# Performance work log

Hardware: AMD Instinct MI355X
Metric: run time of the kernel (lower is better)

The kernel has to match this reference:

```python
import jax, jax.numpy as jnp
import numpy as np

B, T, D = 16, 2048, 1024
TT = T - 2            # tokens after stripping BOS/EOS
WORD_EVERY = 3        # a word starts every 3 BPE tokens
MAX_WORDS = TT // WORD_EVERY  # 682
NUM_MUTEX, NUM_BIN = 64, 32


def setup_inputs() -> dict:
    key = jax.random.key(0)
    ks = jax.random.split(key, 7)
    features = jax.random.normal(ks[0], (B, T, D), dtype=jnp.float32)
    word_starts = jnp.zeros((B, TT), dtype=jnp.int32).at[:, ::WORD_EVERY].set(1)
    s = 1.0 / np.sqrt(D)
    dense_w = jax.random.normal(ks[1], (D, D), dtype=jnp.float32) * s
    dense_b = jax.random.normal(ks[2], (D,), dtype=jnp.float32) * 0.01
    out_w = jax.random.normal(ks[3], (NUM_MUTEX, D), dtype=jnp.float32) * s
    out_b = jax.random.normal(ks[4], (NUM_MUTEX,), dtype=jnp.float32) * 0.01
    bin_w = jax.random.normal(ks[5], (NUM_BIN, D + NUM_MUTEX), dtype=jnp.float32) * s
    bin_b = jax.random.normal(ks[6], (NUM_BIN,), dtype=jnp.float32) * 0.01
    return {"features": features, "word_starts": word_starts,
            "dense_w": dense_w, "dense_b": dense_b,
            "out_w": out_w, "out_b": out_b,
            "bin_w": bin_w, "bin_b": bin_b,
            "max_words": MAX_WORDS}


def _word_features(features, word_starts, max_words):
    # strip BOS/EOS
    x = features[:, 1:-1]                                  # [B, TT, D]
    b, tt, d = x.shape
    seg = jnp.cumsum(word_starts, axis=1) - 1              # word id per token; -1 before first start
    valid = seg >= 0
    flat_seg = seg + jnp.arange(b, dtype=seg.dtype)[:, None] * max_words
    overflow = b * max_words                               # dump invalid tokens into extra bucket
    flat_seg = jnp.where(valid, flat_seg, overflow).reshape(-1)
    sums = jax.ops.segment_sum(x.reshape(-1, d), flat_seg,
                               num_segments=b * max_words + 1)[:-1]
    counts = jax.ops.segment_sum(jnp.ones((b * tt,), dtype=x.dtype), flat_seg,
                                 num_segments=b * max_words + 1)[:-1]
    sums = sums.reshape(b, max_words, d)
    counts = counts.reshape(b, max_words, 1)
    # torch code initializes word_features to ONES; empty slots stay 1.0
    return jnp.where(counts > 0, sums, jnp.ones((), dtype=x.dtype))


def reference(features, word_starts, dense_w, dense_b, out_w, out_b, bin_w, bin_b, max_words):
    wf = _word_features(features, word_starts, max_words)   # [B, MW, D]
    # dropout p=0 (eval) -> identity
    h = jnp.tanh(jnp.einsum('bwd,ed->bwe', wf, dense_w) + dense_b)
    word_class_logits = jnp.einsum('bwd,cd->bwc', h, out_w) + out_b
    cat = jnp.concatenate((word_class_logits, h), axis=-1)  # [B, MW, Cm+D]
    binary_logits = jnp.einsum('bwd,cd->bwc', cat, bin_w) + bin_b
    return (word_class_logits, binary_logits)
```

## Files before the change

kernel.cpp:

```cpp
#include <hip/hip_runtime.h>
#include <stdint.h>

#define B_   16
#define T_   2048
#define D_   1024
#define TT_  2046
#define W_   682
#define BW_  (B_ * W_)
#define NMUT 64
#define NBIN 32

typedef __attribute__((ext_vector_type(8))) short s8b;
typedef __attribute__((ext_vector_type(4))) float f32x4;

__device__ inline short f2bf(float f) {
    uint32_t u = __builtin_bit_cast(uint32_t, f);
    u += 0x7FFFu + ((u >> 16) & 1u);
    return (short)(u >> 16);
}

__device__ inline float fast_tanh(float x) {
    float xc = fminf(fmaxf(x, -15.f), 15.f);
    float e  = __expf(2.f * xc);
    return 1.f - 2.f / (e + 1.f);
}

__device__ inline void gload_lds16(const void* g, void* l) {
    __builtin_amdgcn_global_load_lds(
        (const __attribute__((address_space(1))) uint32_t*)g,
        (__attribute__((address_space(3))) uint32_t*)l, 16, 0, 0);
}

__global__ __launch_bounds__(256) void k_prep(const int* __restrict__ ws,
                                              const float* __restrict__ dw,
                                              const float* __restrict__ ow,
                                              const float* __restrict__ ob,
                                              const float* __restrict__ bw,
                                              const float* __restrict__ bb,
                                              int* __restrict__ starts,
                                              int* __restrict__ nwords,
                                              short* __restrict__ dwb,
                                              short* __restrict__ Bcat,
                                              float* __restrict__ beff) {
    __shared__ float smem[NMUT];
    int blk = blockIdx.x;
    int tid = threadIdx.x;

    if (blk < 16) {
        int b = blk;
        const int* row = ws + (size_t)b * TT_;
        int vals[8], incl[8];
        int p = 0;
        int t0 = tid * 8;
#pragma unroll
        for (int i = 0; i < 8; ++i) {
            int t = t0 + i;
            int v = (t < TT_) ? row[t] : 0;
            vals[i] = v;
            p += v;
            incl[i] = p;
        }
        int tot = p;
        int lane = tid & 63;
        int x = tot;
#pragma unroll
        for (int off = 1; off < 64; off <<= 1) {
            int v = __shfl_up(x, off);
            if (lane >= off) x += v;
        }
        int* wsum = (int*)smem;
        int wid = tid >> 6;
        if (lane == 63) wsum[wid] = x;
        __syncthreads();
        int wbase = 0;
        for (int q = 0; q < wid; ++q) wbase += wsum[q];
        int excl = wbase + x - tot;
        int* st = starts + (size_t)b * (W_ + 1);
#pragma unroll
        for (int i = 0; i < 8; ++i) {
            if (vals[i]) {
                int w = excl + incl[i] - 1;
                if (w <= W_) st[w] = t0 + i;
            }
        }
        if (tid == 0) {
            int total = wsum[0] + wsum[1] + wsum[2] + wsum[3];
            int nw = total < W_ ? total : W_;
            nwords[b] = nw;
            if (total <= W_) st[total] = TT_;
        }
    } else if (blk < 16 + 1024) {
        int i = (blk - 16) * 256 + tid;
        float4 v = ((const float4*)dw)[i];
        short4 o;
        o.x = f2bf(v.x); o.y = f2bf(v.y); o.z = f2bf(v.z); o.w = f2bf(v.w);
        *(short4*)(dwb + (size_t)i * 4) = o;
    } else if (blk < 16 + 1024 + 64) {
        int i = (blk - 1040) * 256 + tid;
        float4 v = ((const float4*)ow)[i];
        short4 o;
        o.x = f2bf(v.x); o.y = f2bf(v.y); o.z = f2bf(v.z); o.w = f2bf(v.w);
        *(short4*)(Bcat + (size_t)i * 4) = o;
    } else {
        int j = blk - 1104;
        if (tid < NMUT) smem[tid] = bw[(size_t)j * (D_ + NMUT) + tid];
        __syncthreads();
        for (int k = tid; k < D_; k += 256) {
            float acc = bw[(size_t)j * (D_ + NMUT) + NMUT + k];
#pragma unroll 8
            for (int c = 0; c < NMUT; ++c)
                acc = fmaf(smem[c], ow[(size_t)c * D_ + k], acc);
            Bcat[(size_t)(NMUT + j) * D_ + k] = f2bf(acc);
        }
        if (tid == 0) {
            float acc = bb[j];
            for (int c = 0; c < NMUT; ++c) acc = fmaf(smem[c], ob[c], acc);
            beff[j] = acc;
        }
    }
}

__global__ __launch_bounds__(256) void k_wf(const float* __restrict__ feat,
                                            const int* __restrict__ starts,
                                            const int* __restrict__ nwords,
                                            short* __restrict__ wf) {
    int blk = blockIdx.x;
    int b = blk / W_;
    int w = blk - b * W_;
    int tid = threadIdx.x;
    short* outp = wf + (size_t)blk * D_ + tid * 4;
    int nw = nwords[b];
    float4 acc = make_float4(0.f, 0.f, 0.f, 0.f);
    if (w >= nw) {
        acc = make_float4(1.f, 1.f, 1.f, 1.f);
    } else {
        const int* st = starts + (size_t)b * (W_ + 1);
        int s = st[w], e = st[w + 1];
        const float4* base = (const float4*)(feat + ((size_t)b * T_ + 1) * D_) + tid;
        for (int t = s; t < e; ++t) {
            float4 v = base[(size_t)t * (D_ / 4)];
            acc.x += v.x; acc.y += v.y; acc.z += v.z; acc.w += v.w;
        }
    }
    short4 o;
    o.x = f2bf(acc.x); o.y = f2bf(acc.y); o.z = f2bf(acc.z); o.w = f2bf(acc.w);
    *(short4*)outp = o;
}

__global__ __launch_bounds__(256) void k_gemm1(const short* __restrict__ wf,
                                               const short* __restrict__ dwb,
                                               const float* __restrict__ db,
                                               short* __restrict__ h) {
    __shared__ short As[2][128 * 32];
    __shared__ short Bs[2][128 * 32];
    int tid  = threadIdx.x;
    int lane = tid & 63;
    int w    = tid >> 6;
    int wm = w >> 1, wn = w & 1;
    int bm = blockIdx.x * 128;
    int bn = blockIdx.y * 128;

    int ln = lane & 15;
    int qk = lane >> 4;

    int srow = lane >> 2;
    int scol = (lane & 3) * 8;

    f32x4 acc[4][4];
#pragma unroll
    for (int i = 0; i < 4; ++i)
#pragma unroll
        for (int j = 0; j < 4; ++j) acc[i][j] = (f32x4){0.f, 0.f, 0.f, 0.f};

    for (int kt = 0; kt < D_; kt += 64) {
#pragma unroll
        for (int hh = 0; hh < 2; ++hh) {
#pragma unroll
            for (int p = 0; p < 2; ++p) {
                int chunk = w * 2 + p;
                int arow = bm + chunk * 16 + srow;
                arow = arow < BW_ ? arow : BW_ - 1;
                gload_lds16(wf + (size_t)arow * D_ + kt + hh * 32 + scol,
                            &As[hh][chunk * 512]);
                int brow = bn + chunk * 16 + srow;
                gload_lds16(dwb + (size_t)brow * D_ + kt + hh * 32 + scol,
                            &Bs[hh][chunk * 512]);
            }
        }
        __syncthreads();
#pragma unroll
        for (int hh = 0; hh < 2; ++hh) {
            s8b af[4], bf[4];
#pragma unroll
            for (int i = 0; i < 4; ++i)
                af[i] = *(const s8b*)&As[hh][(wm * 64 + i * 16 + ln) * 32 + qk * 8];
#pragma unroll
            for (int j = 0; j < 4; ++j)
                bf[j] = *(const s8b*)&Bs[hh][(wn * 64 + j * 16 + ln) * 32 + qk * 8];
#pragma unroll
            for (int i = 0; i < 4; ++i)
#pragma unroll
                for (int j = 0; j < 4; ++j)
                    acc[i][j] = __builtin_amdgcn_mfma_f32_16x16x32_bf16(
                        af[i], bf[j], acc[i][j], 0, 0, 0);
        }
        __syncthreads();
    }

    float bias[4];
#pragma unroll
    for (int j = 0; j < 4; ++j) bias[j] = db[bn + wn * 64 + j * 16 + ln];
#pragma unroll
    for (int i = 0; i < 4; ++i) {
        int row0 = bm + wm * 64 + i * 16 + qk * 4;
#pragma unroll
        for (int r = 0; r < 4; ++r) {
            int row = row0 + r;
            if (row < BW_) {
#pragma unroll
                for (int j = 0; j < 4; ++j) {
                    int cn = bn + wn * 64 + j * 16 + ln;
                    h[(size_t)row * D_ + cn] =
                        f2bf(fast_tanh(acc[i][j][r] + bias[j]));
                }
            }
        }
    }
}

__global__ __launch_bounds__(256) void k_gemm2(const short* __restrict__ h,
                                               const short* __restrict__ Bcat,
                                               const float* __restrict__ ob,
                                               const float* __restrict__ beff,
                                               float* __restrict__ out) {
    int tid  = threadIdx.x;
    int lane = tid & 63;
    int w    = tid >> 6;
    int ln = lane & 15, qk = lane >> 4;
    int m0 = blockIdx.x * 64 + w * 16;

    int arow = m0 + ln;
    arow = arow < BW_ ? arow : BW_ - 1;
    const short* ap = h + (size_t)arow * D_ + qk * 8;
    const short* bp = Bcat + (size_t)ln * D_ + qk * 8;

    f32x4 acc[6];
#pragma unroll
    for (int j = 0; j < 6; ++j) acc[j] = (f32x4){0.f, 0.f, 0.f, 0.f};

#pragma unroll 4
    for (int kt = 0; kt < D_; kt += 32) {
        s8b af = *(const s8b*)(ap + kt);
        s8b bf[6];
#pragma unroll
        for (int j = 0; j < 6; ++j)
            bf[j] = *(const s8b*)(bp + (size_t)j * 16 * D_ + kt);
#pragma unroll
        for (int j = 0; j < 6; ++j)
            acc[j] = __builtin_amdgcn_mfma_f32_16x16x32_bf16(af, bf[j], acc[j], 0, 0, 0);
    }

    float bj[6];
#pragma unroll
    for (int j = 0; j < 6; ++j) {
        int c = j * 16 + ln;
        bj[j] = (c < NMUT) ? ob[c] : beff[c - NMUT];
    }
#pragma unroll
    for (int r = 0; r < 4; ++r) {
        int row = m0 + qk * 4 + r;
        if (row < BW_) {
#pragma unroll
            for (int j = 0; j < 6; ++j) {
                int c = j * 16 + ln;
                float v = acc[j][r] + bj[j];
                if (c < NMUT) out[(size_t)row * NMUT + c] = v;
                else out[(size_t)BW_ * NMUT + (size_t)row * NBIN + (c - NMUT)] = v;
            }
        }
    }
}

extern "C" void kernel_launch(void* const* d_in, const int* in_sizes, int n_in,
                              void* d_out, int out_size, void* d_ws, size_t ws_size,
                              hipStream_t stream) {
    const float* feat    = (const float*)d_in[0];
    const int*   wstarts = (const int*)d_in[1];
    const float* dw      = (const float*)d_in[2];
    const float* db      = (const float*)d_in[3];
    const float* ow      = (const float*)d_in[4];
    const float* ob      = (const float*)d_in[5];
    const float* bw      = (const float*)d_in[6];
    const float* bb      = (const float*)d_in[7];
    float* out = (float*)d_out;

    char* ws = (char*)d_ws;
    size_t off = 0;
    auto alloc = [&](size_t bytes) {
        void* p = ws + off;
        off += (bytes + 255) & ~(size_t)255;
        return p;
    };
    short* wf     = (short*)alloc((size_t)BW_ * D_ * 2);
    short* h      = (short*)alloc((size_t)BW_ * D_ * 2);
    short* dwb    = (short*)alloc((size_t)D_ * D_ * 2);
    short* Bcat   = (short*)alloc((size_t)(NMUT + NBIN) * D_ * 2);
    float* beff   = (float*)alloc(NBIN * 4);
    int*   starts = (int*)alloc((size_t)B_ * (W_ + 1) * 4);
    int*   nwords = (int*)alloc(B_ * 4);

    k_prep<<<1136, 256, 0, stream>>>(wstarts, dw, ow, ob, bw, bb,
                                     starts, nwords, dwb, Bcat, beff);
    k_wf<<<BW_, 256, 0, stream>>>(feat, starts, nwords, wf);
    k_gemm1<<<dim3((BW_ + 127) / 128, D_ / 128), 256, 0, stream>>>(wf, dwb, db, h);
    k_gemm2<<<(BW_ + 63) / 64, 256, 0, stream>>>(h, Bcat, ob, beff, out);
}
```

Baseline: 283.8 us.

## Fuse second GEMM into first GEMM epilogue via LDS tile and atomic accumulation

The tanh tile stays in LDS as bf16. Each gemm1 block multiplies its 128x128 slice by the matching K-slice of the combined output weights and atomically adds the partial logits into the output. The prep kernel now pre-fills the output with the output biases and the folded binary biases. This removes the h write and read and the extra kernel launch, at the cost of 8-way float atomics per output element and a nondeterministic summation order.

```diff
diff --git a/kernel.cpp b/kernel.cpp
--- a/kernel.cpp
+++ b/kernel.cpp
@@ -41,7 +41,7 @@
                                               int* __restrict__ nwords,
                                               short* __restrict__ dwb,
                                               short* __restrict__ Bcat,
-                                              float* __restrict__ beff) {
+                                              float* __restrict__ out) {
     __shared__ float smem[NMUT];
     int blk = blockIdx.x;
     int tid = threadIdx.x;
@@ -95,13 +95,13 @@
         short4 o;
         o.x = f2bf(v.x); o.y = f2bf(v.y); o.z = f2bf(v.z); o.w = f2bf(v.w);
         *(short4*)(dwb + (size_t)i * 4) = o;
-    } else if (blk < 16 + 1024 + 64) {
+    } else if (blk < 1104) {
         int i = (blk - 1040) * 256 + tid;
         float4 v = ((const float4*)ow)[i];
         short4 o;
         o.x = f2bf(v.x); o.y = f2bf(v.y); o.z = f2bf(v.z); o.w = f2bf(v.w);
         *(short4*)(Bcat + (size_t)i * 4) = o;
-    } else {
+    } else if (blk < 1136) {
         int j = blk - 1104;
         if (tid < NMUT) smem[tid] = bw[(size_t)j * (D_ + NMUT) + tid];
         __syncthreads();
@@ -112,11 +112,22 @@
                 acc = fmaf(smem[c], ow[(size_t)c * D_ + k], acc);
             Bcat[(size_t)(NMUT + j) * D_ + k] = f2bf(acc);
         }
-        if (tid == 0) {
-            float acc = bb[j];
-            for (int c = 0; c < NMUT; ++c) acc = fmaf(smem[c], ob[c], acc);
-            beff[j] = acc;
-        }
+    } else if (blk < 1818) {
+        int i4 = (blk - 1136) * 256 + tid;
+        float4 bias = ((const float4*)ob)[i4 & 15];
+        ((float4*)out)[i4] = bias;
+    } else {
+        if (tid < NBIN) {
+            float acc = bb[tid];
+            for (int c = 0; c < NMUT; ++c)
+                acc = fmaf(bw[(size_t)tid * (D_ + NMUT) + c], ob[c], acc);
+            smem[tid] = acc;
+        }
+        __syncthreads();
+        int i4 = (blk - 1818) * 256 + tid;
+        int c4 = (i4 & 7) * 4;
+        float4 bias = make_float4(smem[c4], smem[c4 + 1], smem[c4 + 2], smem[c4 + 3]);
+        ((float4*)(out + (size_t)BW_ * NMUT))[i4] = bias;
     }
 }
 
@@ -147,12 +158,13 @@
     *(short4*)outp = o;
 }
 
+#define CT_STRIDE 136
 __global__ __launch_bounds__(256) void k_gemm1(const short* __restrict__ wf,
                                                const short* __restrict__ dwb,
                                                const float* __restrict__ db,
-                                               short* __restrict__ h) {
-    __shared__ short As[2][128 * 32];
-    __shared__ short Bs[2][128 * 32];
+                                               const short* __restrict__ Bcat,
+                                               float* __restrict__ out) {
+    __shared__ short lds[128 * CT_STRIDE];
     int tid  = threadIdx.x;
     int lane = tid & 63;
     int w    = tid >> 6;
@@ -181,10 +193,10 @@
                 int arow = bm + chunk * 16 + srow;
                 arow = arow < BW_ ? arow : BW_ - 1;
                 gload_lds16(wf + (size_t)arow * D_ + kt + hh * 32 + scol,
-                            &As[hh][chunk * 512]);
+                            &lds[hh * 4096 + chunk * 512]);
                 int brow = bn + chunk * 16 + srow;
                 gload_lds16(dwb + (size_t)brow * D_ + kt + hh * 32 + scol,
-                            &Bs[hh][chunk * 512]);
+                            &lds[8192 + hh * 4096 + chunk * 512]);
             }
         }
         __syncthreads();
@@ -193,10 +205,10 @@
             s8b af[4], bf[4];
 #pragma unroll
             for (int i = 0; i < 4; ++i)
-                af[i] = *(const s8b*)&As[hh][(wm * 64 + i * 16 + ln) * 32 + qk * 8];
+                af[i] = *(const s8b*)&lds[hh * 4096 + (wm * 64 + i * 16 + ln) * 32 + qk * 8];
 #pragma unroll
             for (int j = 0; j < 4; ++j)
-                bf[j] = *(const s8b*)&Bs[hh][(wn * 64 + j * 16 + ln) * 32 + qk * 8];
+                bf[j] = *(const s8b*)&lds[8192 + hh * 4096 + (wn * 64 + j * 16 + ln) * 32 + qk * 8];
 #pragma unroll
             for (int i = 0; i < 4; ++i)
 #pragma unroll
@@ -212,70 +224,56 @@
     for (int j = 0; j < 4; ++j) bias[j] = db[bn + wn * 64 + j * 16 + ln];
 #pragma unroll
     for (int i = 0; i < 4; ++i) {
-        int row0 = bm + wm * 64 + i * 16 + qk * 4;
 #pragma unroll
         for (int r = 0; r < 4; ++r) {
-            int row = row0 + r;
+            int rl = wm * 64 + i * 16 + qk * 4 + r;
+#pragma unroll
+            for (int j = 0; j < 4; ++j) {
+                int cl = wn * 64 + j * 16 + ln;
+                lds[rl * CT_STRIDE + cl] = f2bf(fast_tanh(acc[i][j][r] + bias[j]));
+            }
+        }
+    }
+    __syncthreads();
+
+    int m0w = w * 32;
+    f32x4 acc2[2][6];
+#pragma unroll
+    for (int rb = 0; rb < 2; ++rb)
+#pragma unroll
+        for (int jf = 0; jf < 6; ++jf) acc2[rb][jf] = (f32x4){0.f, 0.f, 0.f, 0.f};
+
+#pragma unroll
+    for (int kc = 0; kc < 4; ++kc) {
+        s8b af2[2], bf2[6];
+#pragma unroll
+        for (int rb = 0; rb < 2; ++rb)
+            af2[rb] = *(const s8b*)&lds[(m0w + rb * 16 + ln) * CT_STRIDE + kc * 32 + qk * 8];
+#pragma unroll
+        for (int jf = 0; jf < 6; ++jf)
+            bf2[jf] = *(const s8b*)(Bcat + (size_t)(jf * 16 + ln) * D_ + bn + kc * 32 + qk * 8);
+#pragma unroll
+        for (int rb = 0; rb < 2; ++rb)
+#pragma unroll
+            for (int jf = 0; jf < 6; ++jf)
+                acc2[rb][jf] = __builtin_amdgcn_mfma_f32_16x16x32_bf16(
+                    af2[rb], bf2[jf], acc2[rb][jf], 0, 0, 0);
+    }
+
+    float* outbin = out + (size_t)BW_ * NMUT;
+#pragma unroll
+    for (int rb = 0; rb < 2; ++rb) {
+#pragma unroll
+        for (int r = 0; r < 4; ++r) {
+            int row = bm + m0w + rb * 16 + qk * 4 + r;
             if (row < BW_) {
 #pragma unroll
-                for (int j = 0; j < 4; ++j) {
-                    int cn = bn + wn * 64 + j * 16 + ln;
-                    h[(size_t)row * D_ + cn] =
-                        f2bf(fast_tanh(acc[i][j][r] + bias[j]));
+                for (int jf = 0; jf < 6; ++jf) {
+                    int c = jf * 16 + ln;
+                    float v = acc2[rb][jf][r];
+                    if (c < NMUT) atomicAdd(out + (size_t)row * NMUT + c, v);
+                    else atomicAdd(outbin + (size_t)row * NBIN + (c - NMUT), v);
                 }
-            }
-        }
-    }
-}
-
-__global__ __launch_bounds__(256) void k_gemm2(const short* __restrict__ h,
-                                               const short* __restrict__ Bcat,
-                                               const float* __restrict__ ob,
-                                               const float* __restrict__ beff,
-                                               float* __restrict__ out) {
-    int tid  = threadIdx.x;
-    int lane = tid & 63;
-    int w    = tid >> 6;
-    int ln = lane & 15, qk = lane >> 4;
-    int m0 = blockIdx.x * 64 + w * 16;
-
-    int arow = m0 + ln;
-    arow = arow < BW_ ? arow : BW_ - 1;
-    const short* ap = h + (size_t)arow * D_ + qk * 8;
-    const short* bp = Bcat + (size_t)ln * D_ + qk * 8;
-
-    f32x4 acc[6];
-#pragma unroll
-    for (int j = 0; j < 6; ++j) acc[j] = (f32x4){0.f, 0.f, 0.f, 0.f};
-
-#pragma unroll 4
-    for (int kt = 0; kt < D_; kt += 32) {
-        s8b af = *(const s8b*)(ap + kt);
-        s8b bf[6];
-#pragma unroll
-        for (int j = 0; j < 6; ++j)
-            bf[j] = *(const s8b*)(bp + (size_t)j * 16 * D_ + kt);
-#pragma unroll
-        for (int j = 0; j < 6; ++j)
-            acc[j] = __builtin_amdgcn_mfma_f32_16x16x32_bf16(af, bf[j], acc[j], 0, 0, 0);
-    }
-
-    float bj[6];
-#pragma unroll
-    for (int j = 0; j < 6; ++j) {
-        int c = j * 16 + ln;
-        bj[j] = (c < NMUT) ? ob[c] : beff[c - NMUT];
-    }
-#pragma unroll
-    for (int r = 0; r < 4; ++r) {
-        int row = m0 + qk * 4 + r;
-        if (row < BW_) {
-#pragma unroll
-            for (int j = 0; j < 6; ++j) {
-                int c = j * 16 + ln;
-                float v = acc[j][r] + bj[j];
-                if (c < NMUT) out[(size_t)row * NMUT + c] = v;
-                else out[(size_t)BW_ * NMUT + (size_t)row * NBIN + (c - NMUT)] = v;
             }
         }
     }
@@ -302,16 +300,13 @@
         return p;
     };
     short* wf     = (short*)alloc((size_t)BW_ * D_ * 2);
-    short* h      = (short*)alloc((size_t)BW_ * D_ * 2);
     short* dwb    = (short*)alloc((size_t)D_ * D_ * 2);
     short* Bcat   = (short*)alloc((size_t)(NMUT + NBIN) * D_ * 2);
-    float* beff   = (float*)alloc(NBIN * 4);
     int*   starts = (int*)alloc((size_t)B_ * (W_ + 1) * 4);
     int*   nwords = (int*)alloc(B_ * 4);
 
-    k_prep<<<1136, 256, 0, stream>>>(wstarts, dw, ow, ob, bw, bb,
-                                     starts, nwords, dwb, Bcat, beff);
+    k_prep<<<2159, 256, 0, stream>>>(wstarts, dw, ow, ob, bw, bb,
+                                     starts, nwords, dwb, Bcat, out);
     k_wf<<<BW_, 256, 0, stream>>>(feat, starts, nwords, wf);
-    k_gemm1<<<dim3((BW_ + 127) / 128, D_ / 128), 256, 0, stream>>>(wf, dwb, db, h);
-    k_gemm2<<<(BW_ + 63) / 64, 256, 0, stream>>>(h, Bcat, ob, beff, out);
-}
+    k_gemm1<<<dim3((BW_ + 127) / 128, D_ / 128), 256, 0, stream>>>(wf, dwb, db, Bcat, out);
+}
```

After: 294.4 us. 1.04x slower.
